# Kernel tuning notes

Measured on AMD Instinct MI355X. Metric: run time of the kernel, lower is better.

The kernel has to match this reference:

```python
import jax, jax.numpy as jnp
import numpy as np

E = 1024
H = 16
D = E // H  # head_dim = 64
L = 2048
S = 2048
N = 2


def setup_inputs() -> dict:
    key = jax.random.key(0)
    ks = jax.random.split(key, 8)
    # xavier_uniform for in_proj_weight: shape (3E, E)
    limit = float(np.sqrt(6.0 / (3 * E + E)))
    in_proj_weight = jax.random.uniform(ks[0], (3 * E, E), jnp.float32, -limit, limit)
    in_proj_bias = jnp.zeros((3 * E,), jnp.float32)
    lim_o = float(np.sqrt(1.0 / E))
    out_w = jax.random.uniform(ks[1], (E, E), jnp.float32, -lim_o, lim_o)
    out_b = jax.random.uniform(ks[2], (E,), jnp.float32, -lim_o, lim_o)
    return {
        "query": jax.random.normal(ks[3], (L, N, E), jnp.float32),
        "key": jax.random.normal(ks[4], (S, N, E), jnp.float32),
        "value": jax.random.normal(ks[5], (S, N, E), jnp.float32),
        "key_padding_mask": jnp.zeros((N, S), bool),
        "attn_mask": jax.random.normal(ks[6], (L, S), jnp.float32),
        "in_proj_weight": in_proj_weight,
        "in_proj_bias": in_proj_bias,
        "out_w": out_w,
        "out_b": out_b,
    }


def reference(query, key, value, key_padding_mask, attn_mask,
              in_proj_weight, in_proj_bias, out_w, out_b):
    # split in_proj into q/k/v slices (rows of the 3E x E weight)
    def proj(base, x):
        W = in_proj_weight[base * E:(base + 1) * E]
        b = in_proj_bias[base * E:(base + 1) * E]
        y = x @ W.T + b  # (T, N, E)
        return y.reshape(y.shape[0], -1, H, D)  # (T, N, H, D)

    q = proj(0, query)   # L,N,H,D
    k = proj(1, key)     # S,N,H,D
    v = proj(2, value)   # S,N,H,D

    logit = jnp.einsum('lnhd,snhd->lnhs', q, k) / jnp.sqrt(jnp.float32(D))
    if key_padding_mask is not None:
        logit = jnp.where(key_padding_mask[None, :, None, :], -jnp.inf, logit)
    if attn_mask is not None:
        logit = logit + attn_mask[:, None, None, :]
    weight = jax.nn.softmax(logit, axis=-1)  # dropout p=0 -> identity
    context = jnp.einsum('lnhs,snhd->lnhd', weight, v)  # L,N,H,D

    context = context.reshape(L, -1, E) @ out_w.T + out_b  # L,N,E
    att = weight.mean(-2).transpose(1, 0, 2)  # N,L,S
    return context, att
```

## Files before the change

### kernel.cpp

```cpp
#include <hip/hip_runtime.h>


#define EDIM   1024
#define HNUM   16
#define DDIM   64
#define LQ     2048
#define SK     2048
#define NBATCH 2

#define NEG_BIG (-3.0e38f)

#define RB  8
#define ST  256
#define NT  (SK/ST)

__device__ __forceinline__ float wave_max_f(float v) {
#pragma unroll
  for (int o = 32; o > 0; o >>= 1) v = fmaxf(v, __shfl_xor(v, o));
  return v;
}
__device__ __forceinline__ float wave_sum_f(float v) {
#pragma unroll
  for (int o = 32; o > 0; o >>= 1) v += __shfl_xor(v, o);
  return v;
}

template <int EPI>
__global__ __launch_bounds__(256) void gemm_k(
    const float* __restrict__ A, const float* __restrict__ W,
    const float* __restrict__ bias, float* __restrict__ C,
    const int M, const int K, const int Nc, const int R)
{
  __shared__ float As[16][132];
  __shared__ float Bs[16][132];
  const int t  = threadIdx.x;
  const int m0 = blockIdx.y * 128;
  const int n0 = blockIdx.x * 128;
  const int lr = t >> 2;
  const int lk = (t & 3) << 2;
  const int tx = t & 15;
  const int ty = t >> 4;

  float acc[2][2][4][4];
#pragma unroll
  for (int a = 0; a < 2; ++a)
#pragma unroll
    for (int b = 0; b < 2; ++b)
#pragma unroll
      for (int i = 0; i < 4; ++i)
#pragma unroll
        for (int j = 0; j < 4; ++j) acc[a][b][i][j] = 0.f;

  float4 ra0, ra1, rb0, rb1;
  ra0 = *(const float4*)&A[(size_t)(m0 + lr) * K + lk];
  ra1 = *(const float4*)&A[(size_t)(m0 + lr + 64) * K + lk];
  rb0 = *(const float4*)&W[(size_t)(n0 + lr) * K + lk];
  rb1 = *(const float4*)&W[(size_t)(n0 + lr + 64) * K + lk];

  for (int k0 = 0; k0 < K; k0 += 16) {
    __syncthreads();
    As[lk+0][lr]    = ra0.x; As[lk+1][lr]    = ra0.y; As[lk+2][lr]    = ra0.z; As[lk+3][lr]    = ra0.w;
    As[lk+0][lr+64] = ra1.x; As[lk+1][lr+64] = ra1.y; As[lk+2][lr+64] = ra1.z; As[lk+3][lr+64] = ra1.w;
    Bs[lk+0][lr]    = rb0.x; Bs[lk+1][lr]    = rb0.y; Bs[lk+2][lr]    = rb0.z; Bs[lk+3][lr]    = rb0.w;
    Bs[lk+0][lr+64] = rb1.x; Bs[lk+1][lr+64] = rb1.y; Bs[lk+2][lr+64] = rb1.z; Bs[lk+3][lr+64] = rb1.w;
    __syncthreads();
    const int kn = k0 + 16;
    if (kn < K) {
      ra0 = *(const float4*)&A[(size_t)(m0 + lr) * K + kn + lk];
      ra1 = *(const float4*)&A[(size_t)(m0 + lr + 64) * K + kn + lk];
      rb0 = *(const float4*)&W[(size_t)(n0 + lr) * K + kn + lk];
      rb1 = *(const float4*)&W[(size_t)(n0 + lr + 64) * K + kn + lk];
    }
#pragma unroll
    for (int kk = 0; kk < 16; ++kk) {
      const float4 a0 = *(const float4*)&As[kk][ty * 4];
      const float4 a1 = *(const float4*)&As[kk][ty * 4 + 64];
      const float4 b0 = *(const float4*)&Bs[kk][tx * 4];
      const float4 b1 = *(const float4*)&Bs[kk][tx * 4 + 64];
      const float av[2][4] = {{a0.x,a0.y,a0.z,a0.w},{a1.x,a1.y,a1.z,a1.w}};
      const float bv[2][4] = {{b0.x,b0.y,b0.z,b0.w},{b1.x,b1.y,b1.z,b1.w}};
#pragma unroll
      for (int qi = 0; qi < 2; ++qi)
#pragma unroll
        for (int i = 0; i < 4; ++i)
#pragma unroll
          for (int qj = 0; qj < 2; ++qj)
#pragma unroll
            for (int j = 0; j < 4; ++j)
              acc[qi][qj][i][j] = fmaf(av[qi][i], bv[qj][j], acc[qi][qj][i][j]);
    }
  }

#pragma unroll
  for (int qi = 0; qi < 2; ++qi)
#pragma unroll
    for (int i = 0; i < 4; ++i) {
      const int gr = m0 + qi * 64 + ty * 4 + i;
      const int row = gr / NBATCH;
      const int nb  = gr % NBATCH;
#pragma unroll
      for (int qj = 0; qj < 2; ++qj)
#pragma unroll
        for (int j = 0; j < 4; ++j) {
          const int gc = n0 + qj * 64 + tx * 4 + j;
          const float val = acc[qi][qj][i][j] + bias[gc];
          if constexpr (EPI == 0) {
            C[(size_t)gr * Nc + gc] = val;
          } else {
            const int h = gc >> 6, d = gc & 63;
            if constexpr (EPI == 1)
              C[(((size_t)nb * HNUM + h) * R + row) * DDIM + d] = val;
            else
              C[(((size_t)nb * HNUM + h) * DDIM + d) * (size_t)R + row] = val;
          }
        }
    }
}

__global__ __launch_bounds__(1024) __attribute__((amdgpu_waves_per_eu(4, 4)))
void attn_k(
    const float* __restrict__ qs, const float* __restrict__ kts,
    const float* __restrict__ vs, const float* __restrict__ amask,
    const unsigned char* __restrict__ kpm,
    float* __restrict__ ctx, float* __restrict__ att)
{
  extern __shared__ float lds[];
  float* p_lds = lds;
  float* kv    = lds + RB * SK;
  float* q_lds = kv + 16384;
  float* part  = q_lds + 512;
  float* red   = part + 2048;
  float* m_l   = red + 32;
  float* ri_l  = m_l + 8;

  const int t    = threadIdx.x;
  const int wg   = blockIdx.x;
  const int n    = wg >> 8;
  const int l0   = (wg & 255) * RB;
  const int wid  = t >> 6;
  const int lane = t & 63;
  const int rr   = t >> 8;
  const int cc   = t & 255;
  const int dd   = t & 63;
  const int sq   = (t >> 6) & 3;

  float attA[NT], attB[NT];
#pragma unroll
  for (int j = 0; j < NT; ++j) { attA[j] = 0.f; attB[j] = 0.f; }

  for (int h = 0; h < HNUM; ++h) {
    const int nh = n * HNUM + h;
    const float* ktb = kts + (size_t)nh * DDIM * SK;
    const float* vb  = vs  + (size_t)nh * SK * DDIM;

    auto kload = [&](int kk, int jj) -> float4 {
      const int i4 = t + kk * 1024;
      return *(const float4*)&ktb[(size_t)(i4 >> 6) * SK + jj * ST + ((i4 & 63) << 2)];
    };
    auto vload = [&](int kk, int jj) -> float4 {
      const int i4 = t + kk * 1024;
      return *(const float4*)&vb[(size_t)(jj * ST + (i4 >> 4)) * DDIM + ((i4 & 15) << 2)];
    };

    float4 pf0 = kload(0, 0), pf1 = kload(1, 0), pf2 = kload(2, 0), pf3 = kload(3, 0);
    float4 qv4;
    if (t < 128) qv4 = ((const float4*)(qs + ((size_t)nh * LQ + l0) * DDIM))[t];
    __syncthreads();
    ((float4*)kv)[t]        = pf0;
    ((float4*)kv)[t + 1024] = pf1;
    ((float4*)kv)[t + 2048] = pf2;
    ((float4*)kv)[t + 3072] = pf3;
    if (t < 128) ((float4*)q_lds)[t] = qv4;
    __syncthreads();

    float rmax0 = NEG_BIG, rmax1 = NEG_BIG;
    const float* qrow0 = q_lds + rr * DDIM;
    const float* qrow1 = q_lds + (rr + 4) * DDIM;

#pragma unroll
    for (int j = 0; j < NT; ++j) {
      if (j < NT - 1) {
        pf0 = kload(0, j + 1); pf1 = kload(1, j + 1);
        pf2 = kload(2, j + 1); pf3 = kload(3, j + 1);
      }
      float a0 = 0.f, b0 = 0.f, a1 = 0.f, b1 = 0.f;
#pragma unroll
      for (int d4 = 0; d4 < DDIM; d4 += 4) {
        const float4 q0 = *(const float4*)&qrow0[d4];
        const float4 q1 = *(const float4*)&qrow1[d4];
        const float k0 = kv[(d4 + 0) * ST + cc];
        const float k1 = kv[(d4 + 1) * ST + cc];
        const float k2 = kv[(d4 + 2) * ST + cc];
        const float k3 = kv[(d4 + 3) * ST + cc];
        a0 = fmaf(q0.x, k0, a0); b0 = fmaf(q0.y, k1, b0);
        a0 = fmaf(q0.z, k2, a0); b0 = fmaf(q0.w, k3, b0);
        a1 = fmaf(q1.x, k0, a1); b1 = fmaf(q1.y, k1, b1);
        a1 = fmaf(q1.z, k2, a1); b1 = fmaf(q1.w, k3, b1);
      }
      const int s = j * ST + cc;
      const bool kill = (kpm[n * SK + s] != 0);
      float l0v = (a0 + b0) * 0.125f + amask[(size_t)(l0 + rr) * SK + s];
      float l1v = (a1 + b1) * 0.125f + amask[(size_t)(l0 + rr + 4) * SK + s];
      if (kill) { l0v = NEG_BIG; l1v = NEG_BIG; }
      p_lds[(size_t)rr * SK + s]       = l0v;
      p_lds[(size_t)(rr + 4) * SK + s] = l1v;
      rmax0 = fmaxf(rmax0, l0v); rmax1 = fmaxf(rmax1, l1v);
      __syncthreads();
      if (j < NT - 1) {
        ((float4*)kv)[t]        = pf0;
        ((float4*)kv)[t + 1024] = pf1;
        ((float4*)kv)[t + 2048] = pf2;
        ((float4*)kv)[t + 3072] = pf3;
        __syncthreads();
      }
    }

    rmax0 = wave_max_f(rmax0); rmax1 = wave_max_f(rmax1);
    if (lane == 0) { red[wid * 2] = rmax0; red[wid * 2 + 1] = rmax1; }
    __syncthreads();
    if (t < RB) {
      const int g = t & 3, ix = t >> 2;
      float m = red[(4 * g) * 2 + ix];
#pragma unroll
      for (int w = 1; w < 4; ++w) m = fmaxf(m, red[(4 * g + w) * 2 + ix]);
      m_l[t] = m;
    }
    __syncthreads();

    const float mm0 = m_l[rr], mm1 = m_l[rr + 4];
    float sum0 = 0.f, sum1 = 0.f;
#pragma unroll
    for (int j = 0; j < NT; ++j) {
      const int s = j * ST + cc;
      const float p0 = __expf(p_lds[(size_t)rr * SK + s] - mm0);
      const float p1 = __expf(p_lds[(size_t)(rr + 4) * SK + s] - mm1);
      p_lds[(size_t)rr * SK + s]       = p0;
      p_lds[(size_t)(rr + 4) * SK + s] = p1;
      sum0 += p0; sum1 += p1;
    }
    sum0 = wave_sum_f(sum0); sum1 = wave_sum_f(sum1);
    if (lane == 0) { red[wid * 2] = sum0; red[wid * 2 + 1] = sum1; }
    __syncthreads();
    if (t < RB) {
      const int g = t & 3, ix = t >> 2;
      float ssum = 0.f;
#pragma unroll
      for (int w = 0; w < 4; ++w) ssum += red[(4 * g + w) * 2 + ix];
      ri_l[t] = 1.0f / ssum;
    }
    __syncthreads();

    const float ri0 = ri_l[rr], ri1 = ri_l[rr + 4];
#pragma unroll
    for (int j = 0; j < NT; ++j) {
      const int s = j * ST + cc;
      attA[j] = fmaf(p_lds[(size_t)rr * SK + s],       ri0, attA[j]);
      attB[j] = fmaf(p_lds[(size_t)(rr + 4) * SK + s], ri1, attB[j]);
    }

    pf0 = vload(0, 0); pf1 = vload(1, 0); pf2 = vload(2, 0); pf3 = vload(3, 0);
    ((float4*)kv)[t]        = pf0;
    ((float4*)kv)[t + 1024] = pf1;
    ((float4*)kv)[t + 2048] = pf2;
    ((float4*)kv)[t + 3072] = pf3;
    __syncthreads();

    float ca00 = 0.f, ca01 = 0.f, ca10 = 0.f, ca11 = 0.f;
#pragma unroll
    for (int j = 0; j < NT; ++j) {
      if (j < NT - 1) {
        pf0 = vload(0, j + 1); pf1 = vload(1, j + 1);
        pf2 = vload(2, j + 1); pf3 = vload(3, j + 1);
      }
      const int sb = sq * 64;
      const float* p0r = p_lds + (size_t)rr * SK + j * ST + sb;
      const float* p1r = p_lds + (size_t)(rr + 4) * SK + j * ST + sb;
#pragma unroll
      for (int s2 = 0; s2 < 64; s2 += 4) {
        const float4 p0 = *(const float4*)&p0r[s2];
        const float4 p1 = *(const float4*)&p1r[s2];
        const float v0 = kv[(sb + s2 + 0) * DDIM + dd];
        const float v1 = kv[(sb + s2 + 1) * DDIM + dd];
        const float v2 = kv[(sb + s2 + 2) * DDIM + dd];
        const float v3 = kv[(sb + s2 + 3) * DDIM + dd];
        ca00 = fmaf(p0.x, v0, ca00); ca01 = fmaf(p0.y, v1, ca01);
        ca00 = fmaf(p0.z, v2, ca00); ca01 = fmaf(p0.w, v3, ca01);
        ca10 = fmaf(p1.x, v0, ca10); ca11 = fmaf(p1.y, v1, ca11);
        ca10 = fmaf(p1.z, v2, ca10); ca11 = fmaf(p1.w, v3, ca11);
      }
      __syncthreads();
      if (j < NT - 1) {
        ((float4*)kv)[t]        = pf0;
        ((float4*)kv)[t + 1024] = pf1;
        ((float4*)kv)[t + 2048] = pf2;
        ((float4*)kv)[t + 3072] = pf3;
        __syncthreads();
      }
    }
    part[(sq * RB + rr) * DDIM + dd]     = ca00 + ca01;
    part[(sq * RB + rr + 4) * DDIM + dd] = ca10 + ca11;
    __syncthreads();
    if (t < RB * DDIM) {
      const int r = t >> 6, d = t & 63;
      float sv = 0.f;
#pragma unroll
      for (int q2 = 0; q2 < 4; ++q2) sv += part[(q2 * RB + r) * DDIM + d];
      ctx[((size_t)(l0 + r) * NBATCH + n) * EDIM + h * DDIM + d] = sv * ri_l[r];
    }
  }

  const float c16 = 1.0f / (float)HNUM;
#pragma unroll
  for (int j = 0; j < NT; ++j) {
    att[((size_t)n * LQ + l0 + rr) * SK + j * ST + cc]     = attA[j] * c16;
    att[((size_t)n * LQ + l0 + rr + 4) * SK + j * ST + cc] = attB[j] * c16;
  }
}

extern "C" void kernel_launch(void* const* d_in, const int* in_sizes, int n_in,
                              void* d_out, int out_size, void* d_ws, size_t ws_size,
                              hipStream_t stream)
{
  const float*         query = (const float*)d_in[0];
  const float*         key   = (const float*)d_in[1];
  const float*         value = (const float*)d_in[2];
  const unsigned char* kpm   = (const unsigned char*)d_in[3];
  const float*         amask = (const float*)d_in[4];
  const float*         ipw   = (const float*)d_in[5];
  const float*         ipb   = (const float*)d_in[6];
  const float*         outw  = (const float*)d_in[7];
  const float*         outb  = (const float*)d_in[8];

  float* outp = (float*)d_out;
  float* att  = outp + (size_t)LQ * NBATCH * EDIM;

  const size_t nQ = (size_t)NBATCH * HNUM * LQ * DDIM;
  const size_t needed = (3 * nQ + (size_t)LQ * NBATCH * EDIM) * 4;
  if (ws_size < needed) return;

  float* ws   = (float*)d_ws;
  float* q_s  = ws;
  float* kt_s = q_s  + nQ;
  float* v_s  = kt_s + nQ;
  float* ctx  = v_s  + nQ;

  const int M = LQ * NBATCH;
  dim3 gg(EDIM / 128, M / 128);

  const int lds_bytes = (RB * SK + 16384 + 512 + 2048 + 32 + 8 + 8) * 4;
  (void)hipFuncSetAttribute((const void*)attn_k,
                            hipFuncAttributeMaxDynamicSharedMemorySize, lds_bytes);

  gemm_k<1><<<gg, 256, 0, stream>>>(query, ipw,                   ipb,            q_s,  M, EDIM, EDIM, LQ);
  gemm_k<2><<<gg, 256, 0, stream>>>(key,   ipw + EDIM * EDIM,     ipb + EDIM,     kt_s, M, EDIM, EDIM, SK);
  gemm_k<1><<<gg, 256, 0, stream>>>(value, ipw + 2 * EDIM * EDIM, ipb + 2 * EDIM, v_s,  M, EDIM, EDIM, SK);
  attn_k<<<NBATCH * (LQ / RB), 1024, lds_bytes, stream>>>(q_s, kt_s, v_s, amask, kpm, ctx, att);
  gemm_k<0><<<gg, 256, 0, stream>>>(ctx, outw, outb, outp, M, EDIM, EDIM, LQ);
}
```

Measured before the change: 2.189 ms.

## Stage K/V/Q tiles via direct global-to-LDS loads in attention kernel

Replaces the register-staged prefetch of K and V tiles (global load into float4 registers, then store to LDS) with the `global_load_lds` builtin, which writes global data straight into LDS. The first V tile is now issued before the softmax reductions so it overlaps them, and the attention-mask and key-padding loads are hoisted ahead of the QK dot product. This cuts VGPR use and LDS store instructions. In exchange, later tiles are issued only after the compute of the current tile finishes, so the previous overlap of the next tile's load with compute is lost and each barrier now waits on the full global latency.

```diff
diff --git a/kernel.cpp b/kernel.cpp
--- a/kernel.cpp
+++ b/kernel.cpp
@@ -23,6 +23,13 @@
 #pragma unroll
   for (int o = 32; o > 0; o >>= 1) v += __shfl_xor(v, o);
   return v;
+}
+
+__device__ __forceinline__ void gll16(const float* g, float* l) {
+  __builtin_amdgcn_global_load_lds(
+      (const __attribute__((address_space(1))) void*)g,
+      (__attribute__((address_space(3))) void*)l,
+      16, 0, 0);
 }
 
 template <int EPI>
@@ -117,8 +124,7 @@
     }
 }
 
-__global__ __launch_bounds__(1024) __attribute__((amdgpu_waves_per_eu(4, 4)))
-void attn_k(
+__global__ __launch_bounds__(1024, 4) void attn_k(
     const float* __restrict__ qs, const float* __restrict__ kts,
     const float* __restrict__ vs, const float* __restrict__ amask,
     const unsigned char* __restrict__ kpm,
@@ -153,24 +159,25 @@
     const float* ktb = kts + (size_t)nh * DDIM * SK;
     const float* vb  = vs  + (size_t)nh * SK * DDIM;
 
-    auto kload = [&](int kk, int jj) -> float4 {
-      const int i4 = t + kk * 1024;
-      return *(const float4*)&ktb[(size_t)(i4 >> 6) * SK + jj * ST + ((i4 & 63) << 2)];
+    auto issueK = [&](int j) {
+#pragma unroll
+      for (int k = 0; k < 4; ++k) {
+        const int d = wid * 4 + k;
+        gll16(ktb + (size_t)d * SK + j * ST + lane * 4, kv + d * ST);
+      }
     };
-    auto vload = [&](int kk, int jj) -> float4 {
-      const int i4 = t + kk * 1024;
-      return *(const float4*)&vb[(size_t)(jj * ST + (i4 >> 4)) * DDIM + ((i4 & 15) << 2)];
+    auto issueV = [&](int j) {
+#pragma unroll
+      for (int k = 0; k < 4; ++k) {
+        const int c = wid * 4 + k;
+        gll16(vb + (size_t)j * (ST * DDIM) + c * 256 + lane * 4, kv + c * 256);
+      }
     };
 
-    float4 pf0 = kload(0, 0), pf1 = kload(1, 0), pf2 = kload(2, 0), pf3 = kload(3, 0);
-    float4 qv4;
-    if (t < 128) qv4 = ((const float4*)(qs + ((size_t)nh * LQ + l0) * DDIM))[t];
-    __syncthreads();
-    ((float4*)kv)[t]        = pf0;
-    ((float4*)kv)[t + 1024] = pf1;
-    ((float4*)kv)[t + 2048] = pf2;
-    ((float4*)kv)[t + 3072] = pf3;
-    if (t < 128) ((float4*)q_lds)[t] = qv4;
+    issueK(0);
+    if (wid < 2)
+      gll16(qs + ((size_t)nh * LQ + l0) * DDIM + wid * 256 + lane * 4,
+            q_lds + wid * 256);
     __syncthreads();
 
     float rmax0 = NEG_BIG, rmax1 = NEG_BIG;
@@ -179,10 +186,10 @@
 
 #pragma unroll
     for (int j = 0; j < NT; ++j) {
-      if (j < NT - 1) {
-        pf0 = kload(0, j + 1); pf1 = kload(1, j + 1);
-        pf2 = kload(2, j + 1); pf3 = kload(3, j + 1);
-      }
+      const int s = j * ST + cc;
+      const float am0 = amask[(size_t)(l0 + rr) * SK + s];
+      const float am1 = amask[(size_t)(l0 + rr + 4) * SK + s];
+      const bool kill = (kpm[n * SK + s] != 0);
       float a0 = 0.f, b0 = 0.f, a1 = 0.f, b1 = 0.f;
 #pragma unroll
       for (int d4 = 0; d4 < DDIM; d4 += 4) {
@@ -197,23 +204,20 @@
         a1 = fmaf(q1.x, k0, a1); b1 = fmaf(q1.y, k1, b1);
         a1 = fmaf(q1.z, k2, a1); b1 = fmaf(q1.w, k3, b1);
       }
-      const int s = j * ST + cc;
-      const bool kill = (kpm[n * SK + s] != 0);
-      float l0v = (a0 + b0) * 0.125f + amask[(size_t)(l0 + rr) * SK + s];
-      float l1v = (a1 + b1) * 0.125f + amask[(size_t)(l0 + rr + 4) * SK + s];
+      float l0v = (a0 + b0) * 0.125f + am0;
+      float l1v = (a1 + b1) * 0.125f + am1;
       if (kill) { l0v = NEG_BIG; l1v = NEG_BIG; }
       p_lds[(size_t)rr * SK + s]       = l0v;
       p_lds[(size_t)(rr + 4) * SK + s] = l1v;
       rmax0 = fmaxf(rmax0, l0v); rmax1 = fmaxf(rmax1, l1v);
       __syncthreads();
       if (j < NT - 1) {
-        ((float4*)kv)[t]        = pf0;
-        ((float4*)kv)[t + 1024] = pf1;
-        ((float4*)kv)[t + 2048] = pf2;
-        ((float4*)kv)[t + 3072] = pf3;
+        issueK(j + 1);
         __syncthreads();
       }
     }
+
+    issueV(0);
 
     rmax0 = wave_max_f(rmax0); rmax1 = wave_max_f(rmax1);
     if (lane == 0) { red[wid * 2] = rmax0; red[wid * 2 + 1] = rmax1; }
@@ -258,20 +262,9 @@
       attB[j] = fmaf(p_lds[(size_t)(rr + 4) * SK + s], ri1, attB[j]);
     }
 
-    pf0 = vload(0, 0); pf1 = vload(1, 0); pf2 = vload(2, 0); pf3 = vload(3, 0);
-    ((float4*)kv)[t]        = pf0;
-    ((float4*)kv)[t + 1024] = pf1;
-    ((float4*)kv)[t + 2048] = pf2;
-    ((float4*)kv)[t + 3072] = pf3;
-    __syncthreads();
-
     float ca00 = 0.f, ca01 = 0.f, ca10 = 0.f, ca11 = 0.f;
 #pragma unroll
     for (int j = 0; j < NT; ++j) {
-      if (j < NT - 1) {
-        pf0 = vload(0, j + 1); pf1 = vload(1, j + 1);
-        pf2 = vload(2, j + 1); pf3 = vload(3, j + 1);
-      }
       const int sb = sq * 64;
       const float* p0r = p_lds + (size_t)rr * SK + j * ST + sb;
       const float* p1r = p_lds + (size_t)(rr + 4) * SK + j * ST + sb;
@@ -290,10 +283,7 @@
       }
       __syncthreads();
       if (j < NT - 1) {
-        ((float4*)kv)[t]        = pf0;
-        ((float4*)kv)[t + 1024] = pf1;
-        ((float4*)kv)[t + 2048] = pf2;
-        ((float4*)kv)[t + 3072] = pf3;
+        issueV(j + 1);
         __syncthreads();
       }
     }
```

After: 2.499 ms. +14.1%, slower.
